# Kernel tuning notes

Hardware: AMD Instinct MI355X
Metric: run time of the kernel (lower is better)

The kernel has to match this reference:

```python
import jax, jax.numpy as jnp
import numpy as np

IN_F, HID, OUT_F = 227, 1024, 227
BATCH, SEQ_LEN = 256, 100
COND_NUM, GT_NUM = 5, 5


def _condition_lst(seq_len, condition_num=COND_NUM, groundtruth_num=GT_NUM):
    gt = np.ones((100, groundtruth_num))
    con = np.zeros((100, condition_num))
    lst = np.concatenate((gt, con), 1).reshape(-1)
    return lst[:seq_len].astype(bool)


def _lstm_cell(x, h, c, Wih, Whh, bih, bhh):
    gates = x @ Wih.T + bih + h @ Whh.T + bhh  # [B, 4H]
    i, f, g, o = jnp.split(gates, 4, axis=-1)
    c_new = jax.nn.sigmoid(f) * c + jax.nn.sigmoid(i) * jnp.tanh(g)
    h_new = jax.nn.sigmoid(o) * jnp.tanh(c_new)
    return h_new, c_new


def setup_inputs() -> dict:
    key = jax.random.key(0)
    ks = jax.random.split(key, 16)
    s = 0.03
    inp = {"real_seq": jax.random.normal(ks[0], (BATCH, SEQ_LEN, IN_F), jnp.float32)}
    shapes = {
        "Wih1": (4 * HID, IN_F), "Whh1": (4 * HID, HID), "bih1": (4 * HID,), "bhh1": (4 * HID,),
        "Wih2": (4 * HID, HID), "Whh2": (4 * HID, HID), "bih2": (4 * HID,), "bhh2": (4 * HID,),
        "Wih3": (4 * HID, HID), "Whh3": (4 * HID, HID), "bih3": (4 * HID,), "bhh3": (4 * HID,),
        "Wd": (OUT_F, HID), "bd": (OUT_F,),
    }
    for i, (name, shp) in enumerate(shapes.items()):
        inp[name] = jax.random.normal(ks[i + 1], shp, jnp.float32) * s
    return inp


def reference(real_seq, Wih1, Whh1, bih1, bhh1, Wih2, Whh2, bih2, bhh2,
              Wih3, Whh3, bih3, bhh3, Wd, bd):
    batch, seq_len, _ = real_seq.shape
    cond = jnp.asarray(_condition_lst(seq_len))  # [T] bool, True -> teacher forcing
    zeros_h = jnp.zeros((batch, HID), real_seq.dtype)
    out0 = jnp.zeros((batch, OUT_F), real_seq.dtype)
    carry0 = (zeros_h, zeros_h, zeros_h, zeros_h, zeros_h, zeros_h, out0)

    def step(carry, xs):
        h0, h1, h2, c0, c1, c2, prev_out = carry
        gt_frame, use_gt = xs
        in_frame = jnp.where(use_gt, gt_frame, prev_out)
        # NOTE: faithful to the original quirk — lstm2/lstm3 consume the OLD
        # h0 / h1 (pre-update), not the freshly computed ones.
        h0n, c0n = _lstm_cell(in_frame, h0, c0, Wih1, Whh1, bih1, bhh1)
        h1n, c1n = _lstm_cell(h0, h1, c1, Wih2, Whh2, bih2, bhh2)
        h2n, c2n = _lstm_cell(h1, h2, c2, Wih3, Whh3, bih3, bhh3)
        out_frame = h2n @ Wd.T + bd
        return (h0n, h1n, h2n, c0n, c1n, c2n, out_frame), out_frame

    xs = (jnp.transpose(real_seq, (1, 0, 2)), cond)  # [T,B,F], [T]
    _, out_frames = jax.lax.scan(step, carry0, xs)   # [T,B,OUT_F]
    out_seq = jnp.transpose(out_frames, (1, 0, 2)).reshape(batch, seq_len * OUT_F)
    return out_seq
```

## Files before the change

kernel.cpp:

```cpp
#include <hip/hip_runtime.h>
#include <cstdint>

typedef _Float16 f16;
typedef _Float16 f16x8 __attribute__((ext_vector_type(8)));
typedef float    f32x4 __attribute__((ext_vector_type(4)));

#define DINL __device__ __forceinline__

static constexpr int HID = 1024;
static constexpr int NG  = 4096;
static constexpr int BB  = 256;
static constexpr int TT  = 100;
static constexpr int KX  = 256;
static constexpr size_t MSZ = (size_t)NG * HID;

static constexpr size_t OFF_PACKW5 = 0;
static constexpr size_t OFF_W1D    = OFF_PACKW5 + 5*MSZ*2;
static constexpr size_t OFF_WIH1   = OFF_W1D   + MSZ*2;
static constexpr size_t OFF_WD     = OFF_WIH1  + (size_t)NG*KX*2;
static constexpr size_t OFF_XPAD   = OFF_WD    + (size_t)256*HID*2;
static constexpr size_t OFF_BIAS   = OFF_XPAD  + (size_t)TT*BB*KX*2;
static constexpr size_t OFF_C      = OFF_BIAS  + (size_t)4*NG*4;
static constexpr size_t OFF_HBUF   = OFF_C     + (size_t)3*BB*HID*4;
static constexpr size_t OFF_H2Z    = OFF_HBUF  + (size_t)4*BB*HID*2;
static constexpr size_t OFF_H2ALL  = OFF_H2Z   + (size_t)BB*HID*2;

DINL size_t fpo(int n, int k, int NCH){
  return ((((size_t)(n>>4)*NCH + (k>>6))*2 + ((k>>5)&1)) << 9)
       + ((size_t)((n&15) | (((k>>3)&3) << 4)) << 3) + (k&7);
}

DINL void async16(void* lds, const void* g){
  auto lp = reinterpret_cast<__attribute__((address_space(3))) unsigned int*>(
      reinterpret_cast<uintptr_t>(lds));
  auto gp = reinterpret_cast<const __attribute__((address_space(1))) unsigned int*>(
      reinterpret_cast<uintptr_t>(g));
  __builtin_amdgcn_global_load_lds(gp, lp, 16, 0, 0);
}

DINL f16x8 ldsr128(unsigned a){
  f16x8 r;
  asm volatile("ds_read_b128 %0, %1" : "=v"(r) : "v"(a));
  return r;
}

DINL f16x8 gload(const void* addr){
  f16x8 r;
  asm volatile("global_load_dwordx4 %0, %1, off"
    : "=v"(r) : "v"(addr));
  return r;
}

DINL f32x4 mfma8(f16x8 a, f16x8 b, f32x4 c){
  return __builtin_amdgcn_mfma_f32_16x16x32_f16(a, b, c, 0, 0, 0);
}

DINL float sigf(float x){
  x = fminf(fmaxf(x, -30.f), 30.f);
  return __fdividef(1.f, 1.f + __expf(-x));
}
DINL float tanh_fast(float x){
  x = fminf(fmaxf(x, -15.f), 15.f);
  float t = __expf(2.f*x);
  return __fdividef(t - 1.f, t + 1.f);
}


__global__ void k_pack5(const float* W0, const float* W1, const float* W2,
                        const float* W3, const float* W4, char* ws)
{
  f16* dst = (f16*)(ws + OFF_PACKW5);
  const int mat = blockIdx.y;
  const float* src = mat==0?W0 : mat==1?W1 : mat==2?W2 : mat==3?W3 : W4;
  int tid = blockIdx.x*256 + threadIdx.x;
  int n = tid >> 7, kc = tid & 127;
  int r = ((n&3) << 10) + (n >> 2);
  const float* s = src + (size_t)r*HID + kc*8;
  f16x8 o;
  #pragma unroll
  for (int i = 0; i < 8; i++) o[i] = (f16)s[i];
  int nt = n >> 4, cch = kc >> 3, kw = (kc >> 2) & 1, quad = kc & 3;
  size_t off = ((((size_t)nt*16 + cch)*2 + kw) << 9)
             + ((size_t)((n&15) | (quad<<4)) << 3);
  *(f16x8*)(dst + (size_t)mat*MSZ + off) = o;
}

__global__ void k_packwih1(const float* __restrict__ Wih1, char* ws){
  f16* dst = (f16*)(ws + OFF_WIH1);
  int n = blockIdx.x, k = threadIdx.x;
  int r = ((n&3) << 10) + (n >> 2);
  dst[fpo(n, k, 4)] = (k < 227) ? (f16)Wih1[(size_t)r*227 + k] : (f16)0.f;
}

__global__ void k_packwd(const float* __restrict__ Wd, char* ws){
  f16* dst = (f16*)(ws + OFF_WD);
  int idx = blockIdx.x*256 + threadIdx.x;
  int o = idx >> 7, k8 = idx & 127;
  f16x8 v;
  #pragma unroll
  for (int e = 0; e < 8; e++)
    v[e] = (o < 227) ? (f16)Wd[(size_t)o*HID + k8*8 + e] : (f16)0.f;
  size_t off = ((((size_t)(o>>4)*16 + (k8>>3))*2 + ((k8>>2)&1)) << 9)
             + ((size_t)((o&15) | ((k8&3)<<4)) << 3);
  *(f16x8*)(dst + off) = v;
}

__global__ void k_packwdt(const float* __restrict__ Wd, char* ws){
  f16* dst = (f16*)(ws + OFF_H2ALL);
  int h = blockIdx.x, o = threadIdx.x;
  dst[fpo(h, o, 4)] = (o < 227) ? (f16)Wd[(size_t)o*HID + h] : (f16)0.f;
}

__global__ void k_xpad(const float* __restrict__ seq, char* ws){
  f16* dst = (f16*)(ws + OFF_XPAD);
  int idx = blockIdx.x*256 + threadIdx.x;
  int t = idx >> 13, rem = idx & 8191, b = rem >> 5, k8 = rem & 31;
  f16x8 v;
  #pragma unroll
  for (int e = 0; e < 8; e++){
    int k = k8*8 + e;
    v[e] = (k < 227) ? (f16)seq[(size_t)b*22700 + (size_t)t*227 + k] : (f16)0.f;
  }
  size_t off = ((((size_t)(b>>4)*4 + (k8>>3))*2 + ((k8>>2)&1)) << 9)
             + ((size_t)((b&15) | ((k8&3)<<4)) << 3);
  *(f16x8*)(dst + (size_t)t*BB*KX + off) = v;
}

__global__ void k_bias(const float* bih1, const float* bhh1, const float* bih2, const float* bhh2,
                       const float* bih3, const float* bhh3, const float* Wih1, const float* bd,
                       char* ws)
{
  int n = blockIdx.x*256 + threadIdx.x;
  if (n >= NG) return;
  int r = ((n&3) << 10) + (n >> 2);
  float* b = (float*)(ws + OFF_BIAS);
  float bf = bih1[r] + bhh1[r];
  float s = 0.f;
  for (int o = 0; o < 227; o++) s += Wih1[(size_t)r*227 + o] * bd[o];
  b[n]        = bf;
  b[NG + n]   = bf + s;
  b[2*NG + n] = bih2[r] + bhh2[r];
  b[3*NG + n] = bih3[r] + bhh3[r];
}

__global__ __launch_bounds__(256) void k_w1d(char* ws)
{
  const int w = threadIdx.x >> 6, lane = threadIdx.x & 63;
  const int n0 = blockIdx.x*128, m0 = blockIdx.y*128;
  const f16* Af = (const f16*)(ws + OFF_WIH1);
  const f16* Bf = (const f16*)(ws + OFF_H2ALL);
  f16* W1D = (f16*)(ws + OFF_W1D);
  const int m_w = m0 + (w>>1)*64, n_w = n0 + (w&1)*64;
  const int vl = lane*8;

  f32x4 acc[4][4];
  f32x4 zero = {0.f, 0.f, 0.f, 0.f};
  #pragma unroll
  for (int i = 0; i < 4; i++)
    #pragma unroll
    for (int j = 0; j < 4; j++) acc[i][j] = zero;

  for (int c = 0; c < 4; c++){
    f16x8 av[4][2], bv[4][2];
    #pragma unroll
    for (int ti = 0; ti < 4; ti++)
      #pragma unroll
      for (int kw = 0; kw < 2; kw++)
        av[ti][kw] = *(const f16x8*)(Af + ((((size_t)((m_w>>4)+ti)*4 + c)*2 + kw) << 9) + vl);
    #pragma unroll
    for (int tj = 0; tj < 4; tj++)
      #pragma unroll
      for (int kw = 0; kw < 2; kw++)
        bv[tj][kw] = *(const f16x8*)(Bf + ((((size_t)((n_w>>4)+tj)*4 + c)*2 + kw) << 9) + vl);
    #pragma unroll
    for (int kw = 0; kw < 2; kw++)
      #pragma unroll
      for (int ti = 0; ti < 4; ti++)
        #pragma unroll
        for (int tj = 0; tj < 4; tj++)
          acc[ti][tj] = mfma8(av[ti][kw], bv[tj][kw], acc[ti][tj]);
  }

  const int quad = lane>>4, c15 = lane&15;
  #pragma unroll
  for (int tj = 0; tj < 4; tj++){
    int col = n_w + tj*16 + c15;
    #pragma unroll
    for (int ti = 0; ti < 4; ti++){
      f32x4 v = acc[ti][tj];
      #pragma unroll
      for (int r = 0; r < 4; r++){
        int m = m_w + ti*16 + quad*4 + r;
        W1D[fpo(m, col, 16)] = (f16)v[r];
      }
    }
  }
}

__global__ __launch_bounds__(512, 2) void k_step(char* __restrict__ ws, int t, int use_gt)
{
  __shared__ __align__(16) char lds[65536];
  const int w = threadIdx.x >> 6, lane = threadIdx.x & 63;
  const int col0 = blockIdx.x*64, layer = blockIdx.y;

  const f16* packW = (const f16*)(ws + OFF_PACKW5);
  const f16* W1D   = (const f16*)(ws + OFF_W1D);
  const f16* WIH1  = (const f16*)(ws + OFF_WIH1);
  const f16* XP    = (const f16*)(ws + OFF_XPAD) + (size_t)t*BB*KX;
  const float* biasb = (const float*)(ws + OFF_BIAS);
  float* Cst = (float*)(ws + OFF_C);
  f16* HB  = (f16*)(ws + OFF_HBUF);
  f16* H2Z = (f16*)(ws + OFF_H2Z);
  f16* H2A = (f16*)(ws + OFF_H2ALL);

  const int pr = t & 1, pw = pr ^ 1;
  const f16* h0p = HB + (size_t)(pr*2 + 0)*BB*HID;
  const f16* h1p = HB + (size_t)(pr*2 + 1)*BB*HID;
  const f16* h2p = (t == 0) ? H2Z : (H2A + (size_t)(t-1)*BB*HID);

  const f16 *A0, *A1, *B0, *B1; int K1;
  const float* biasp; f16* hout; float* cptr;
  if (layer == 0){
    A0 = h0p; B0 = packW;
    if (use_gt){ A1 = XP;  B1 = WIH1; K1 = KX;  biasp = biasb; }
    else       { A1 = h2p; B1 = W1D;  K1 = HID; biasp = biasb + NG; }
    hout = HB + (size_t)(pw*2 + 0)*BB*HID; cptr = Cst;
  } else if (layer == 1){
    A0 = h0p; B0 = packW + MSZ;  A1 = h1p; B1 = packW + 2*MSZ; K1 = HID;
    biasp = biasb + 2*NG; hout = HB + (size_t)(pw*2 + 1)*BB*HID; cptr = Cst + (size_t)BB*HID;
  } else {
    A0 = h1p; B0 = packW + 3*MSZ; A1 = h2p; B1 = packW + 4*MSZ; K1 = HID;
    biasp = biasb + 3*NG; hout = H2A + (size_t)t*BB*HID; cptr = Cst + (size_t)2*BB*HID;
  }
  const int ncmax = 16 + (K1 >> 6);
  const int NCH1  = K1 >> 6;

  const int m_w = w*32, c15 = lane&15, quad = lane>>4;
  const unsigned vl16 = (unsigned)(lane * 16);
  const unsigned ldsBase = (unsigned)(uintptr_t)lds;

  const char* a0b[2]; const char* a1b[2];
  #pragma unroll
  for (int ti = 0; ti < 2; ti++){
    a0b[ti] = (const char*)A0 + (size_t)(2*w + ti)*16*2048   + (size_t)lane*16;
    a1b[ti] = (const char*)A1 + (size_t)(2*w + ti)*NCH1*2048 + (size_t)lane*16;
  }
  const char* b0u = (const char*)B0 + (size_t)((col0>>4) + (w>>1))*16*2048   + (size_t)(w&1)*1024 + (size_t)lane*16;
  const char* b1u = (const char*)B1 + (size_t)((col0>>4) + (w>>1))*NCH1*2048 + (size_t)(w&1)*1024 + (size_t)lane*16;

  auto issueB = [&](int ci){
    const char* s = (ci < 16) ? (b0u + (size_t)ci*2048) : (b1u + (size_t)(ci-16)*2048);
    async16(lds + (ci & 7)*8192 + w*1024, s);
  };
  auto abase = [&](int ci, int ti)->const char*{
    return (ci < 16) ? (a0b[ti] + (size_t)ci*2048) : (a1b[ti] + (size_t)(ci-16)*2048);
  };

  f32x4 acc[2][4];
  f32x4 zero = {0.f, 0.f, 0.f, 0.f};
  #pragma unroll
  for (int i = 0; i < 2; i++)
    #pragma unroll
    for (int j = 0; j < 4; j++) acc[i][j] = zero;

  f16x8 A0r[4], A1r[4], A2r[4];
  f16x8 F0[8], F1[8];

#define ISSUEA(CI, AK)                                           \
  { const char* _b0 = abase((CI), 0);                            \
    const char* _b1 = abase((CI), 1);                            \
    AK[0] = gload(_b0);                                          \
    AK[1] = gload(_b0 + 1024);                                   \
    AK[2] = gload(_b1);                                          \
    AK[3] = gload(_b1 + 1024); }

#define WAITA_N(LIT, AK) asm volatile("s_waitcnt vmcnt(" #LIT ")" \
    : "+v"(AK[0]), "+v"(AK[1]), "+v"(AK[2]), "+v"(AK[3]))

#define DS8(CI, F)                                               \
  { const unsigned _sb = ldsBase + (unsigned)(((CI)&7)*8192) + vl16; \
    F[0] = ldsr128(_sb);         F[1] = ldsr128(_sb + 1024u);    \
    F[2] = ldsr128(_sb + 2048u); F[3] = ldsr128(_sb + 3072u);    \
    F[4] = ldsr128(_sb + 4096u); F[5] = ldsr128(_sb + 5120u);    \
    F[6] = ldsr128(_sb + 6144u); F[7] = ldsr128(_sb + 7168u); }

#define LGKM_N(LIT, F) asm volatile("s_waitcnt lgkmcnt(" #LIT ")" \
    : "+v"(F[0]), "+v"(F[1]), "+v"(F[2]), "+v"(F[3]),            \
      "+v"(F[4]), "+v"(F[5]), "+v"(F[6]), "+v"(F[7]))

#define MFMA16(AK, F)                                            \
    acc[0][0] = mfma8(AK[0], F[0], acc[0][0]);                   \
    acc[0][1] = mfma8(AK[0], F[2], acc[0][1]);                   \
    acc[0][2] = mfma8(AK[0], F[4], acc[0][2]);                   \
    acc[0][3] = mfma8(AK[0], F[6], acc[0][3]);                   \
    acc[1][0] = mfma8(AK[2], F[0], acc[1][0]);                   \
    acc[1][1] = mfma8(AK[2], F[2], acc[1][1]);                   \
    acc[1][2] = mfma8(AK[2], F[4], acc[1][2]);                   \
    acc[1][3] = mfma8(AK[2], F[6], acc[1][3]);                   \
    acc[0][0] = mfma8(AK[1], F[1], acc[0][0]);                   \
    acc[0][1] = mfma8(AK[1], F[3], acc[0][1]);                   \
    acc[0][2] = mfma8(AK[1], F[5], acc[0][2]);                   \
    acc[0][3] = mfma8(AK[1], F[7], acc[0][3]);                   \
    acc[1][0] = mfma8(AK[3], F[1], acc[1][0]);                   \
    acc[1][1] = mfma8(AK[3], F[3], acc[1][1]);                   \
    acc[1][2] = mfma8(AK[3], F[5], acc[1][2]);                   \
    acc[1][3] = mfma8(AK[3], F[7], acc[1][3]);

#define BARRIER_ { __builtin_amdgcn_s_barrier(); __builtin_amdgcn_sched_barrier(0); }
#define ISSUEB4(G) { const int _cb = 4*(G); issueB(_cb); issueB(_cb+1); issueB(_cb+2); issueB(_cb+3); }

  ISSUEB4(0); ISSUEB4(1);
  ISSUEA(0, A0r); ISSUEA(1, A1r); ISSUEA(2, A2r);
  asm volatile("s_waitcnt vmcnt(16)" ::: "memory");
  BARRIER_;
  DS8(0, F0);

  WAITA_N(8, A0r); DS8(1, F1); LGKM_N(8, F0); MFMA16(A0r, F0); ISSUEA(3, A0r);
  WAITA_N(8, A1r); DS8(2, F0); LGKM_N(8, F1); MFMA16(A1r, F1); ISSUEA(4, A1r);
  WAITA_N(8, A2r); DS8(3, F1); LGKM_N(8, F0); MFMA16(A2r, F0); ISSUEA(5, A2r);

  const int nblk = (ncmax - 8) / 12;
  for (int blk = 0; blk < nblk; ++blk){
    const int c0 = 3 + 12*blk, g0 = c0 >> 2;
    LGKM_N(0, F1); BARRIER_; ISSUEB4(g0+2);
    WAITA_N(12, A0r); DS8(c0+1, F0); MFMA16(A0r, F1); ISSUEA(c0+3, A0r);
    WAITA_N(12, A1r); DS8(c0+2, F1); LGKM_N(8, F0); MFMA16(A1r, F0); ISSUEA(c0+4,  A1r);
    WAITA_N(12, A2r); DS8(c0+3, F0); LGKM_N(8, F1); MFMA16(A2r, F1); ISSUEA(c0+5,  A2r);
    WAITA_N(8,  A0r); DS8(c0+4, F1); LGKM_N(8, F0); MFMA16(A0r, F0); ISSUEA(c0+6,  A0r);
    LGKM_N(0, F1); BARRIER_; ISSUEB4(g0+3);
    WAITA_N(12, A1r); DS8(c0+5, F0); MFMA16(A1r, F1); ISSUEA(c0+7, A1r);
    WAITA_N(12, A2r); DS8(c0+6, F1); LGKM_N(8, F0); MFMA16(A2r, F0); ISSUEA(c0+8,  A2r);
    WAITA_N(12, A0r); DS8(c0+7, F0); LGKM_N(8, F1); MFMA16(A0r, F1); ISSUEA(c0+9,  A0r);
    WAITA_N(8,  A1r); DS8(c0+8, F1); LGKM_N(8, F0); MFMA16(A1r, F0); ISSUEA(c0+10, A1r);
    LGKM_N(0, F1); BARRIER_; ISSUEB4(g0+4);
    WAITA_N(12, A2r); DS8(c0+9, F0); MFMA16(A2r, F1); ISSUEA(c0+11, A2r);
    WAITA_N(12, A0r); DS8(c0+10, F1); LGKM_N(8, F0); MFMA16(A0r, F0); ISSUEA(c0+12, A0r);
    WAITA_N(12, A1r); DS8(c0+11, F0); LGKM_N(8, F1); MFMA16(A1r, F1); ISSUEA(c0+13, A1r);
    WAITA_N(8,  A2r); DS8(c0+12, F1); LGKM_N(8, F0); MFMA16(A2r, F0); ISSUEA(c0+14, A2r);
  }

  LGKM_N(0, F1); BARRIER_;
  WAITA_N(8, A0r); DS8(ncmax-4, F0); MFMA16(A0r, F1); ISSUEA(ncmax-2, A0r);
  WAITA_N(8, A1r); DS8(ncmax-3, F1); LGKM_N(8, F0); MFMA16(A1r, F0); ISSUEA(ncmax-1, A1r);
  WAITA_N(8, A2r); DS8(ncmax-2, F0); LGKM_N(8, F1); MFMA16(A2r, F1);
  WAITA_N(4, A0r); DS8(ncmax-1, F1); LGKM_N(8, F0); MFMA16(A0r, F0);
  WAITA_N(0, A1r);                   LGKM_N(0, F1); MFMA16(A1r, F1);

#undef ISSUEB4
#undef BARRIER_
#undef MFMA16
#undef LGKM_N
#undef DS8
#undef WAITA_N
#undef ISSUEA

  const int gl = lane&3, sbase = lane&60;
  #pragma unroll
  for (int tj = 0; tj < 4; tj++){
    const int ncol = col0 + tj*16 + c15;
    const int unit = ncol >> 2;
    const float bn = biasp[ncol];
    float cp[8];
    #pragma unroll
    for (int ti = 0; ti < 2; ti++)
      #pragma unroll
      for (int r = 0; r < 4; r++)
        cp[ti*4 + r] = cptr[(size_t)(m_w + ti*16 + quad*4 + r)*HID + unit];
    #pragma unroll
    for (int ti = 0; ti < 2; ti++){
      f32x4 v = acc[ti][tj];
      #pragma unroll
      for (int r = 0; r < 4; r++){
        float x   = v[r] + bn;
        float act = (gl == 2) ? tanh_fast(x) : sigf(x);
        float iv = __shfl(act, sbase);
        float fv = __shfl(act, sbase + 1);
        float gv = __shfl(act, sbase + 2);
        float ov = __shfl(act, sbase + 3);
        float cn = fmaf(fv, cp[ti*4 + r], iv*gv);
        float hn = ov * tanh_fast(cn);
        int m = m_w + ti*16 + quad*4 + r;
        if (gl == 0)      cptr[(size_t)m*HID + unit] = cn;
        else if (gl == 1) hout[fpo(m, unit, 16)] = (f16)hn;
      }
    }
  }
}

__global__ __launch_bounds__(256) void k_final(const char* __restrict__ ws,
                                               const float* __restrict__ bd,
                                               float* __restrict__ dout)
{
  const int w = threadIdx.x >> 6, lane = threadIdx.x & 63;
  const int n0 = blockIdx.x*128, m0 = blockIdx.y*128;
  const char* Bf = ws + OFF_WD;
  const int m_w = m0 + (w>>1)*64, n_w = n0 + (w&1)*64;
  const char* Af = ws + OFF_H2ALL + (size_t)(m_w >> 8)*BB*HID*2;
  const int vl = lane*16;

  f32x4 acc[4][4];
  f32x4 zero = {0.f, 0.f, 0.f, 0.f};
  #pragma unroll
  for (int i = 0; i < 4; i++)
    #pragma unroll
    for (int j = 0; j < 4; j++) acc[i][j] = zero;

  for (int c = 0; c < 16; c++){
    f16x8 av[4][2], bv[4][2];
    #pragma unroll
    for (int ti = 0; ti < 4; ti++){
      const char* b = Af + (((size_t)(((m_w & 255) >> 4) + ti)*16 + c) << 11) + vl;
      av[ti][0] = *(const f16x8*)(b);
      av[ti][1] = *(const f16x8*)(b + 1024);
    }
    #pragma unroll
    for (int tj = 0; tj < 4; tj++){
      const char* b = Bf + (((size_t)((n_w >> 4) + tj)*16 + c) << 11) + vl;
      bv[tj][0] = *(const f16x8*)(b);
      bv[tj][1] = *(const f16x8*)(b + 1024);
    }
    #pragma unroll
    for (int kw = 0; kw < 2; kw++)
      #pragma unroll
      for (int ti = 0; ti < 4; ti++)
        #pragma unroll
        for (int tj = 0; tj < 4; tj++)
          acc[ti][tj] = mfma8(av[ti][kw], bv[tj][kw], acc[ti][tj]);
  }

  const int quad = lane>>4, c15 = lane&15;
  #pragma unroll
  for (int tj = 0; tj < 4; tj++){
    int o = n_w + tj*16 + c15;
    bool valid = (o < 227);
    float bn = valid ? bd[o] : 0.f;
    #pragma unroll
    for (int ti = 0; ti < 4; ti++){
      f32x4 v = acc[ti][tj];
      #pragma unroll
      for (int r = 0; r < 4; r++){
        int m = m_w + ti*16 + quad*4 + r;
        if (valid){
          int tt = m >> 8, b = m & 255;
          dout[(size_t)b*22700 + (size_t)tt*227 + o] = v[r] + bn;
        }
      }
    }
  }
}

extern "C" void kernel_launch(void* const* d_in, const int* in_sizes, int n_in,
                              void* d_out, int out_size, void* d_ws, size_t ws_size,
                              hipStream_t stream)
{
  (void)in_sizes; (void)n_in; (void)out_size; (void)ws_size;
  const float* seq  = (const float*)d_in[0];
  const float* Wih1 = (const float*)d_in[1];
  const float* Whh1 = (const float*)d_in[2];
  const float* bih1 = (const float*)d_in[3];
  const float* bhh1 = (const float*)d_in[4];
  const float* Wih2 = (const float*)d_in[5];
  const float* Whh2 = (const float*)d_in[6];
  const float* bih2 = (const float*)d_in[7];
  const float* bhh2 = (const float*)d_in[8];
  const float* Wih3 = (const float*)d_in[9];
  const float* Whh3 = (const float*)d_in[10];
  const float* bih3 = (const float*)d_in[11];
  const float* bhh3 = (const float*)d_in[12];
  const float* Wd   = (const float*)d_in[13];
  const float* bd   = (const float*)d_in[14];
  char* ws = (char*)d_ws;

  (void)hipMemsetAsync(ws + OFF_C,    0, (size_t)3*BB*HID*4, stream);
  (void)hipMemsetAsync(ws + OFF_HBUF, 0, (size_t)2*BB*HID*2, stream);
  (void)hipMemsetAsync(ws + OFF_H2Z,  0, (size_t)BB*HID*2,   stream);

  k_pack5   <<<dim3(2048, 5), dim3(256), 0, stream>>>(Whh1, Wih2, Whh2, Wih3, Whh3, ws);
  k_packwih1<<<dim3(4096),    dim3(256), 0, stream>>>(Wih1, ws);
  k_packwd  <<<dim3(128),     dim3(256), 0, stream>>>(Wd, ws);
  k_packwdt <<<dim3(1024),    dim3(256), 0, stream>>>(Wd, ws);
  k_xpad    <<<dim3(3200),    dim3(256), 0, stream>>>(seq, ws);
  k_bias    <<<dim3(16),      dim3(256), 0, stream>>>(bih1, bhh1, bih2, bhh2, bih3, bhh3, Wih1, bd, ws);
  k_w1d     <<<dim3(8, 32),   dim3(256), 0, stream>>>(ws);

  for (int t = 0; t < TT; t++){
    int ug = ((t % 10) < 5) ? 1 : 0;
    k_step<<<dim3(64, 3), dim3(512), 0, stream>>>(ws, t, ug);
  }

  k_final<<<dim3(2, 200), dim3(256), 0, stream>>>((const char*)ws, bd, (float*)d_out);
}
```

Baseline: 2.880 ms.

## Fuse per-timestep launches into one persistent cooperative kernel with atomic barriers

```diff
diff --git a/kernel.cpp b/kernel.cpp
--- a/kernel.cpp
+++ b/kernel.cpp
@@ -197,7 +197,7 @@
   }
 }
 
-__global__ __launch_bounds__(512, 2) void k_step(char* __restrict__ ws, int t, int use_gt)
+__global__ __launch_bounds__(512, 1) void k_steps(char* __restrict__ ws)
 {
   __shared__ __align__(16) char lds[65536];
   const int w = threadIdx.x >> 6, lane = threadIdx.x & 63;
@@ -206,65 +206,108 @@
   const f16* packW = (const f16*)(ws + OFF_PACKW5);
   const f16* W1D   = (const f16*)(ws + OFF_W1D);
   const f16* WIH1  = (const f16*)(ws + OFF_WIH1);
-  const f16* XP    = (const f16*)(ws + OFF_XPAD) + (size_t)t*BB*KX;
+  const f16* XPb   = (const f16*)(ws + OFF_XPAD);
   const float* biasb = (const float*)(ws + OFF_BIAS);
-  float* Cst = (float*)(ws + OFF_C);
+  unsigned* arrive = (unsigned*)(ws + OFF_C);
   f16* HB  = (f16*)(ws + OFF_HBUF);
   f16* H2Z = (f16*)(ws + OFF_H2Z);
   f16* H2A = (f16*)(ws + OFF_H2ALL);
 
-  const int pr = t & 1, pw = pr ^ 1;
-  const f16* h0p = HB + (size_t)(pr*2 + 0)*BB*HID;
-  const f16* h1p = HB + (size_t)(pr*2 + 1)*BB*HID;
-  const f16* h2p = (t == 0) ? H2Z : (H2A + (size_t)(t-1)*BB*HID);
-
-  const f16 *A0, *A1, *B0, *B1; int K1;
-  const float* biasp; f16* hout; float* cptr;
-  if (layer == 0){
-    A0 = h0p; B0 = packW;
-    if (use_gt){ A1 = XP;  B1 = WIH1; K1 = KX;  biasp = biasb; }
-    else       { A1 = h2p; B1 = W1D;  K1 = HID; biasp = biasb + NG; }
-    hout = HB + (size_t)(pw*2 + 0)*BB*HID; cptr = Cst;
-  } else if (layer == 1){
-    A0 = h0p; B0 = packW + MSZ;  A1 = h1p; B1 = packW + 2*MSZ; K1 = HID;
-    biasp = biasb + 2*NG; hout = HB + (size_t)(pw*2 + 1)*BB*HID; cptr = Cst + (size_t)BB*HID;
-  } else {
-    A0 = h1p; B0 = packW + 3*MSZ; A1 = h2p; B1 = packW + 4*MSZ; K1 = HID;
-    biasp = biasb + 3*NG; hout = H2A + (size_t)t*BB*HID; cptr = Cst + (size_t)2*BB*HID;
-  }
-  const int ncmax = 16 + (K1 >> 6);
-  const int NCH1  = K1 >> 6;
+  const f16* B0  = (layer==0) ? packW : (layer==1) ? packW + MSZ : packW + 3*MSZ;
+  const f16* B1n = (layer==0) ? W1D   : (layer==1) ? packW + 2*MSZ : packW + 4*MSZ;
 
   const int m_w = w*32, c15 = lane&15, quad = lane>>4;
   const unsigned vl16 = (unsigned)(lane * 16);
   const unsigned ldsBase = (unsigned)(uintptr_t)lds;
 
-  const char* a0b[2]; const char* a1b[2];
-  #pragma unroll
-  for (int ti = 0; ti < 2; ti++){
-    a0b[ti] = (const char*)A0 + (size_t)(2*w + ti)*16*2048   + (size_t)lane*16;
-    a1b[ti] = (const char*)A1 + (size_t)(2*w + ti)*NCH1*2048 + (size_t)lane*16;
-  }
-  const char* b0u = (const char*)B0 + (size_t)((col0>>4) + (w>>1))*16*2048   + (size_t)(w&1)*1024 + (size_t)lane*16;
-  const char* b1u = (const char*)B1 + (size_t)((col0>>4) + (w>>1))*NCH1*2048 + (size_t)(w&1)*1024 + (size_t)lane*16;
-
-  auto issueB = [&](int ci){
-    const char* s = (ci < 16) ? (b0u + (size_t)ci*2048) : (b1u + (size_t)(ci-16)*2048);
-    async16(lds + (ci & 7)*8192 + w*1024, s);
-  };
-  auto abase = [&](int ci, int ti)->const char*{
-    return (ci < 16) ? (a0b[ti] + (size_t)ci*2048) : (a1b[ti] + (size_t)(ci-16)*2048);
-  };
-
-  f32x4 acc[2][4];
+  const char* b0u   = (const char*)B0  + (size_t)((col0>>4) + (w>>1))*16*2048 + (size_t)(w&1)*1024 + (size_t)lane*16;
+  const char* b1u_n = (const char*)B1n + (size_t)((col0>>4) + (w>>1))*16*2048 + (size_t)(w&1)*1024 + (size_t)lane*16;
+  const char* b1u_g = (const char*)WIH1 + (size_t)((col0>>4) + (w>>1))*4*2048 + (size_t)(w&1)*1024 + (size_t)lane*16;
+
+  const float* bsel0 = (layer==0) ? biasb      : (layer==1) ? biasb + 2*NG : biasb + 3*NG;
+  const float* bsel1 = (layer==0) ? biasb + NG : bsel0;
+  float bgt[4], bngt[4];
+  #pragma unroll
+  for (int tj = 0; tj < 4; tj++){
+    int ncol = col0 + tj*16 + c15;
+    bgt[tj]  = bsel0[ncol];
+    bngt[tj] = bsel1[ncol];
+  }
+
+  float creg[32];
+  #pragma unroll
+  for (int i = 0; i < 32; i++) creg[i] = 0.f;
+
   f32x4 zero = {0.f, 0.f, 0.f, 0.f};
-  #pragma unroll
-  for (int i = 0; i < 2; i++)
-    #pragma unroll
-    for (int j = 0; j < 4; j++) acc[i][j] = zero;
-
   f16x8 A0r[4], A1r[4], A2r[4];
   f16x8 F0[8], F1[8];
+
+  auto prefetchB01 = [&](){
+    #pragma unroll
+    for (int k = 0; k < 8; k++)
+      async16(lds + k*8192 + w*1024, b0u + (size_t)k*2048);
+  };
+
+  prefetchB01();
+
+  for (int t = 0; t < TT; ++t){
+    const int use_gt = ((t % 10) < 5) ? 1 : 0;
+    const int pr = t & 1, pw = pr ^ 1;
+    const f16* h0p = HB + (size_t)(pr*2 + 0)*BB*HID;
+    const f16* h1p = HB + (size_t)(pr*2 + 1)*BB*HID;
+    const f16* h2p = (t == 0) ? H2Z : (H2A + (size_t)(t-1)*BB*HID);
+
+    const f16 *A0, *A1; const char* b1u; int NCH1; f16* hout;
+    if (layer == 0){
+      A0 = h0p;
+      if (use_gt){ A1 = XPb + (size_t)t*BB*KX; b1u = b1u_g; NCH1 = 4;  }
+      else       { A1 = h2p;                   b1u = b1u_n; NCH1 = 16; }
+      hout = HB + (size_t)(pw*2 + 0)*BB*HID;
+    } else if (layer == 1){
+      A0 = h0p; A1 = h1p; b1u = b1u_n; NCH1 = 16;
+      hout = HB + (size_t)(pw*2 + 1)*BB*HID;
+    } else {
+      A0 = h1p; A1 = h2p; b1u = b1u_n; NCH1 = 16;
+      hout = H2A + (size_t)t*BB*HID;
+    }
+    const int ncmax = 16 + NCH1;
+    const int nblk  = (ncmax - 8) / 12;
+
+    if (t > 0){
+      const unsigned needv = 64u * (unsigned)t;
+      if (threadIdx.x < 3){
+        const int idx = threadIdx.x;
+        bool req = (layer == 0) ? (idx < 2 || !use_gt)
+                 : (layer == 1) ? true : (idx >= 1);
+        if (req){
+          while (__hip_atomic_load(&arrive[idx*32], __ATOMIC_RELAXED,
+                                   __HIP_MEMORY_SCOPE_AGENT) < needv)
+            __builtin_amdgcn_s_sleep(2);
+        }
+      }
+      __syncthreads();
+      __threadfence();
+    }
+
+    const char* a0b[2]; const char* a1b[2];
+    #pragma unroll
+    for (int ti = 0; ti < 2; ti++){
+      a0b[ti] = (const char*)A0 + (size_t)(2*w + ti)*16*2048   + (size_t)lane*16;
+      a1b[ti] = (const char*)A1 + (size_t)(2*w + ti)*NCH1*2048 + (size_t)lane*16;
+    }
+    auto issueB = [&](int ci){
+      const char* s = (ci < 16) ? (b0u + (size_t)ci*2048) : (b1u + (size_t)(ci-16)*2048);
+      async16(lds + (ci & 7)*8192 + w*1024, s);
+    };
+    auto abase = [&](int ci, int ti)->const char*{
+      return (ci < 16) ? (a0b[ti] + (size_t)ci*2048) : (a1b[ti] + (size_t)(ci-16)*2048);
+    };
+
+    f32x4 acc[2][4];
+    #pragma unroll
+    for (int i = 0; i < 2; i++)
+      #pragma unroll
+      for (int j = 0; j < 4; j++) acc[i][j] = zero;
 
 #define ISSUEA(CI, AK)                                           \
   { const char* _b0 = abase((CI), 0);                            \
@@ -309,42 +352,40 @@
 #define BARRIER_ { __builtin_amdgcn_s_barrier(); __builtin_amdgcn_sched_barrier(0); }
 #define ISSUEB4(G) { const int _cb = 4*(G); issueB(_cb); issueB(_cb+1); issueB(_cb+2); issueB(_cb+3); }
 
-  ISSUEB4(0); ISSUEB4(1);
-  ISSUEA(0, A0r); ISSUEA(1, A1r); ISSUEA(2, A2r);
-  asm volatile("s_waitcnt vmcnt(16)" ::: "memory");
-  BARRIER_;
-  DS8(0, F0);
-
-  WAITA_N(8, A0r); DS8(1, F1); LGKM_N(8, F0); MFMA16(A0r, F0); ISSUEA(3, A0r);
-  WAITA_N(8, A1r); DS8(2, F0); LGKM_N(8, F1); MFMA16(A1r, F1); ISSUEA(4, A1r);
-  WAITA_N(8, A2r); DS8(3, F1); LGKM_N(8, F0); MFMA16(A2r, F0); ISSUEA(5, A2r);
-
-  const int nblk = (ncmax - 8) / 12;
-  for (int blk = 0; blk < nblk; ++blk){
-    const int c0 = 3 + 12*blk, g0 = c0 >> 2;
-    LGKM_N(0, F1); BARRIER_; ISSUEB4(g0+2);
-    WAITA_N(12, A0r); DS8(c0+1, F0); MFMA16(A0r, F1); ISSUEA(c0+3, A0r);
-    WAITA_N(12, A1r); DS8(c0+2, F1); LGKM_N(8, F0); MFMA16(A1r, F0); ISSUEA(c0+4,  A1r);
-    WAITA_N(12, A2r); DS8(c0+3, F0); LGKM_N(8, F1); MFMA16(A2r, F1); ISSUEA(c0+5,  A2r);
-    WAITA_N(8,  A0r); DS8(c0+4, F1); LGKM_N(8, F0); MFMA16(A0r, F0); ISSUEA(c0+6,  A0r);
-    LGKM_N(0, F1); BARRIER_; ISSUEB4(g0+3);
-    WAITA_N(12, A1r); DS8(c0+5, F0); MFMA16(A1r, F1); ISSUEA(c0+7, A1r);
-    WAITA_N(12, A2r); DS8(c0+6, F1); LGKM_N(8, F0); MFMA16(A2r, F0); ISSUEA(c0+8,  A2r);
-    WAITA_N(12, A0r); DS8(c0+7, F0); LGKM_N(8, F1); MFMA16(A0r, F1); ISSUEA(c0+9,  A0r);
-    WAITA_N(8,  A1r); DS8(c0+8, F1); LGKM_N(8, F0); MFMA16(A1r, F0); ISSUEA(c0+10, A1r);
-    LGKM_N(0, F1); BARRIER_; ISSUEB4(g0+4);
-    WAITA_N(12, A2r); DS8(c0+9, F0); MFMA16(A2r, F1); ISSUEA(c0+11, A2r);
-    WAITA_N(12, A0r); DS8(c0+10, F1); LGKM_N(8, F0); MFMA16(A0r, F0); ISSUEA(c0+12, A0r);
-    WAITA_N(12, A1r); DS8(c0+11, F0); LGKM_N(8, F1); MFMA16(A1r, F1); ISSUEA(c0+13, A1r);
-    WAITA_N(8,  A2r); DS8(c0+12, F1); LGKM_N(8, F0); MFMA16(A2r, F0); ISSUEA(c0+14, A2r);
-  }
-
-  LGKM_N(0, F1); BARRIER_;
-  WAITA_N(8, A0r); DS8(ncmax-4, F0); MFMA16(A0r, F1); ISSUEA(ncmax-2, A0r);
-  WAITA_N(8, A1r); DS8(ncmax-3, F1); LGKM_N(8, F0); MFMA16(A1r, F0); ISSUEA(ncmax-1, A1r);
-  WAITA_N(8, A2r); DS8(ncmax-2, F0); LGKM_N(8, F1); MFMA16(A2r, F1);
-  WAITA_N(4, A0r); DS8(ncmax-1, F1); LGKM_N(8, F0); MFMA16(A0r, F0);
-  WAITA_N(0, A1r);                   LGKM_N(0, F1); MFMA16(A1r, F1);
+    ISSUEA(0, A0r); ISSUEA(1, A1r); ISSUEA(2, A2r);
+    asm volatile("s_waitcnt vmcnt(16)" ::: "memory");
+    BARRIER_;
+    DS8(0, F0);
+
+    WAITA_N(8, A0r); DS8(1, F1); LGKM_N(8, F0); MFMA16(A0r, F0); ISSUEA(3, A0r);
+    WAITA_N(8, A1r); DS8(2, F0); LGKM_N(8, F1); MFMA16(A1r, F1); ISSUEA(4, A1r);
+    WAITA_N(8, A2r); DS8(3, F1); LGKM_N(8, F0); MFMA16(A2r, F0); ISSUEA(5, A2r);
+
+    for (int blk = 0; blk < nblk; ++blk){
+      const int c0 = 3 + 12*blk, g0 = c0 >> 2;
+      LGKM_N(0, F1); BARRIER_; ISSUEB4(g0+2);
+      WAITA_N(12, A0r); DS8(c0+1, F0); MFMA16(A0r, F1); ISSUEA(c0+3, A0r);
+      WAITA_N(12, A1r); DS8(c0+2, F1); LGKM_N(8, F0); MFMA16(A1r, F0); ISSUEA(c0+4,  A1r);
+      WAITA_N(12, A2r); DS8(c0+3, F0); LGKM_N(8, F1); MFMA16(A2r, F1); ISSUEA(c0+5,  A2r);
+      WAITA_N(8,  A0r); DS8(c0+4, F1); LGKM_N(8, F0); MFMA16(A0r, F0); ISSUEA(c0+6,  A0r);
+      LGKM_N(0, F1); BARRIER_; ISSUEB4(g0+3);
+      WAITA_N(12, A1r); DS8(c0+5, F0); MFMA16(A1r, F1); ISSUEA(c0+7, A1r);
+      WAITA_N(12, A2r); DS8(c0+6, F1); LGKM_N(8, F0); MFMA16(A2r, F0); ISSUEA(c0+8,  A2r);
+      WAITA_N(12, A0r); DS8(c0+7, F0); LGKM_N(8, F1); MFMA16(A0r, F1); ISSUEA(c0+9,  A0r);
+      WAITA_N(8,  A1r); DS8(c0+8, F1); LGKM_N(8, F0); MFMA16(A1r, F0); ISSUEA(c0+10, A1r);
+      LGKM_N(0, F1); BARRIER_; ISSUEB4(g0+4);
+      WAITA_N(12, A2r); DS8(c0+9, F0); MFMA16(A2r, F1); ISSUEA(c0+11, A2r);
+      WAITA_N(12, A0r); DS8(c0+10, F1); LGKM_N(8, F0); MFMA16(A0r, F0); ISSUEA(c0+12, A0r);
+      WAITA_N(12, A1r); DS8(c0+11, F0); LGKM_N(8, F1); MFMA16(A1r, F1); ISSUEA(c0+13, A1r);
+      WAITA_N(8,  A2r); DS8(c0+12, F1); LGKM_N(8, F0); MFMA16(A2r, F0); ISSUEA(c0+14, A2r);
+    }
+
+    LGKM_N(0, F1); BARRIER_;
+    WAITA_N(8, A0r); DS8(ncmax-4, F0); MFMA16(A0r, F1); ISSUEA(ncmax-2, A0r);
+    WAITA_N(8, A1r); DS8(ncmax-3, F1); LGKM_N(8, F0); MFMA16(A1r, F0); ISSUEA(ncmax-1, A1r);
+    WAITA_N(8, A2r); DS8(ncmax-2, F0); LGKM_N(8, F1); MFMA16(A2r, F1);
+    WAITA_N(4, A0r); DS8(ncmax-1, F1); LGKM_N(8, F0); MFMA16(A0r, F0);
+    WAITA_N(0, A1r);                   LGKM_N(0, F1); MFMA16(A1r, F1);
 
 #undef ISSUEB4
 #undef BARRIER_
@@ -354,36 +395,38 @@
 #undef WAITA_N
 #undef ISSUEA
 
-  const int gl = lane&3, sbase = lane&60;
-  #pragma unroll
-  for (int tj = 0; tj < 4; tj++){
-    const int ncol = col0 + tj*16 + c15;
-    const int unit = ncol >> 2;
-    const float bn = biasp[ncol];
-    float cp[8];
-    #pragma unroll
-    for (int ti = 0; ti < 2; ti++)
-      #pragma unroll
-      for (int r = 0; r < 4; r++)
-        cp[ti*4 + r] = cptr[(size_t)(m_w + ti*16 + quad*4 + r)*HID + unit];
-    #pragma unroll
-    for (int ti = 0; ti < 2; ti++){
-      f32x4 v = acc[ti][tj];
-      #pragma unroll
-      for (int r = 0; r < 4; r++){
-        float x   = v[r] + bn;
-        float act = (gl == 2) ? tanh_fast(x) : sigf(x);
-        float iv = __shfl(act, sbase);
-        float fv = __shfl(act, sbase + 1);
-        float gv = __shfl(act, sbase + 2);
-        float ov = __shfl(act, sbase + 3);
-        float cn = fmaf(fv, cp[ti*4 + r], iv*gv);
-        float hn = ov * tanh_fast(cn);
-        int m = m_w + ti*16 + quad*4 + r;
-        if (gl == 0)      cptr[(size_t)m*HID + unit] = cn;
-        else if (gl == 1) hout[fpo(m, unit, 16)] = (f16)hn;
+    const int gl = lane&3, sbase = lane&60;
+    #pragma unroll
+    for (int tj = 0; tj < 4; tj++){
+      const int ncol = col0 + tj*16 + c15;
+      const int unit = ncol >> 2;
+      const float bn = use_gt ? bgt[tj] : bngt[tj];
+      #pragma unroll
+      for (int ti = 0; ti < 2; ti++){
+        f32x4 v = acc[ti][tj];
+        #pragma unroll
+        for (int r = 0; r < 4; r++){
+          float x   = v[r] + bn;
+          float act = (gl == 2) ? tanh_fast(x) : sigf(x);
+          float iv = __shfl(act, sbase);
+          float fv = __shfl(act, sbase + 1);
+          float gv = __shfl(act, sbase + 2);
+          float ov = __shfl(act, sbase + 3);
+          float cn = fmaf(fv, creg[tj*8 + ti*4 + r], iv*gv);
+          creg[tj*8 + ti*4 + r] = cn;
+          float hn = ov * tanh_fast(cn);
+          int m = m_w + ti*16 + quad*4 + r;
+          if (gl == 1) hout[fpo(m, unit, 16)] = (f16)hn;
+        }
       }
     }
+
+    __threadfence();
+    __syncthreads();
+    if (threadIdx.x == 0)
+      __hip_atomic_fetch_add(&arrive[layer*32], 1u, __ATOMIC_RELAXED,
+                             __HIP_MEMORY_SCOPE_AGENT);
+    if (t + 1 < TT) prefetchB01();
   }
 }
 
@@ -483,10 +526,9 @@
   k_bias    <<<dim3(16),      dim3(256), 0, stream>>>(bih1, bhh1, bih2, bhh2, bih3, bhh3, Wih1, bd, ws);
   k_w1d     <<<dim3(8, 32),   dim3(256), 0, stream>>>(ws);
 
-  for (int t = 0; t < TT; t++){
-    int ug = ((t % 10) < 5) ? 1 : 0;
-    k_step<<<dim3(64, 3), dim3(512), 0, stream>>>(ws, t, ug);
-  }
+  char* wsp = ws;
+  void* kargs[] = { (void*)&wsp };
+  (void)hipLaunchCooperativeKernel((const void*)k_steps, dim3(64, 3), dim3(512), kargs, 0, stream);
 
   k_final<<<dim3(2, 200), dim3(256), 0, stream>>>((const char*)ws, bd, (float*)d_out);
 }
```

Result: slower. 9.371 ms (+225.4%).
